# Kernel tuning notes

Measured on AMD Instinct MI355X. Metric: run time of the kernel, lower is better.

Reference implementation:

```python
import jax, jax.numpy as jnp
import numpy as np

ORDER = 2
M = 3  # number_timeseries


def setup_inputs() -> dict:
    key = jax.random.key(0)
    ks = jax.random.split(key, 8)
    N, T = 256, 4096
    H, OUT = 128, 10
    d_phi_in = (ORDER + 1) * M          # 9
    d_rho_in = ORDER * M + H            # 134
    s = lambda fan_in: 1.0 / np.sqrt(fan_in)
    return {
        "x": jax.random.normal(ks[0], (N, M * T), dtype=jnp.float32),
        "phi_w1": jax.random.normal(ks[1], (d_phi_in, H), dtype=jnp.float32) * s(d_phi_in),
        "phi_b1": jnp.zeros((H,), jnp.float32),
        "phi_w2": jax.random.normal(ks[2], (H, H), dtype=jnp.float32) * s(H),
        "phi_b2": jnp.zeros((H,), jnp.float32),
        "phi_w3": jax.random.normal(ks[3], (H, H), dtype=jnp.float32) * s(H),
        "phi_b3": jnp.zeros((H,), jnp.float32),
        "rho_w1": jax.random.normal(ks[4], (d_rho_in, H), dtype=jnp.float32) * s(d_rho_in),
        "rho_b1": jnp.zeros((H,), jnp.float32),
        "rho_w2": jax.random.normal(ks[5], (H, OUT), dtype=jnp.float32) * s(H),
        "rho_b2": jnp.zeros((OUT,), jnp.float32),
    }


def reference(x, phi_w1, phi_b1, phi_w2, phi_b2, phi_w3, phi_b3,
              rho_w1, rho_b1, rho_w2, rho_b2):
    N = x.shape[0]
    xr = x.reshape(N, M, -1)                      # (N, M, T)
    T = xr.shape[-1]
    L = T - ORDER                                 # number of windows
    # cat over lags along channel dim, then transpose -> (N, L, (ORDER+1)*M)
    input_inner = jnp.concatenate(
        [xr[:, :, i:L + i] for i in range(ORDER + 1)], axis=1
    ).swapaxes(1, 2)                              # (N, L, 9)
    h = jax.nn.relu(input_inner @ phi_w1 + phi_b1)
    h = jax.nn.relu(h @ phi_w2 + phi_b2)
    h = h @ phi_w3 + phi_b3                       # (N, L, 128)
    output_inner = jnp.sum(h, axis=1)             # (N, 128)
    input_outer = jnp.concatenate(
        [xr[:, :, :ORDER].reshape(N, -1), output_inner], axis=1
    )                                             # (N, 134)
    g = jax.nn.relu(input_outer @ rho_w1 + rho_b1)
    return g @ rho_w2 + rho_b2                    # (N, 10)
```

## Files before the change

kernel.cpp:

```cpp
#include <hip/hip_runtime.h>
#include <hip/hip_bf16.h>


#define NN 256
#define MM 3
#define TT 4096
#define LL 4094
#define HH 128
#define CHUNKS 8
#define RPC 512
#define RPH 256
#define HALVES 2
#define STEPS 4
#define SR 64
#define XROW 24

typedef __attribute__((ext_vector_type(8))) short bf16x8;
typedef __attribute__((ext_vector_type(4))) float f32x4;
typedef __attribute__((ext_vector_type(4))) unsigned short u16x4;
typedef __attribute__((ext_vector_type(2))) unsigned int u32x2;

__device__ __forceinline__ unsigned short f2bf(float x) {
    __hip_bfloat16 h = __float2bfloat16(x);
    union { __hip_bfloat16 h; unsigned short u; } v; v.h = h;
    return v.u;
}

__global__ __launch_bounds__(256, 4) void pen_inner(
    const float* __restrict__ x,
    const float* __restrict__ w1, const float* __restrict__ b1,
    const float* __restrict__ w2, const float* __restrict__ b2,
    float* __restrict__ partials)
{
    __shared__ __align__(16) unsigned short xw[XROW * (RPH + 1) + 8];
    __shared__ __align__(16) unsigned short h1s[SR * HH];

    const int tid  = threadIdx.x;
    const int wave = tid >> 6;
    const int lane = tid & 63;
    const int lr   = lane & 15;
    const int lq   = lane >> 4;

    const int bx    = blockIdx.x;
    const int n     = bx >> 3;
    const int chunk = bx & 7;
    const int l0c   = chunk * RPC;

    const float* xn = x + n * (MM * TT);

    const int fo0 = wave * 2;
    bf16x8 w1f[2];
    bf16x8 w2f[2][4];
    f32x4  b1f[2], b2f[2];
    #pragma unroll
    for (int f = 0; f < 2; ++f) {
        const int c = (fo0 + f) * 16 + lr;
        bf16x8 a;
        #pragma unroll
        for (int e = 0; e < 8; ++e) {
            int k = lq * 8 + e;
            a[e] = (short)((k < 9) ? f2bf(w1[k * HH + c]) : (unsigned short)0);
        }
        w1f[f] = a;
        #pragma unroll
        for (int kk = 0; kk < 4; ++kk) {
            bf16x8 wv;
            #pragma unroll
            for (int e = 0; e < 8; ++e)
                wv[e] = (short)f2bf(w2[(kk * 32 + lq * 8 + e) * HH + c]);
            w2f[f][kk] = wv;
        }
        #pragma unroll
        for (int j = 0; j < 4; ++j) {
            b1f[f][j] = b1[(fo0 + f) * 16 + lq * 4 + j];
            b2f[f][j] = b2[(fo0 + f) * 16 + lq * 4 + j];
        }
    }

    if (tid < XROW + 8) xw[XROW * RPH + tid] = 0;

    const int xo = XROW * lr + 8 * lq;

    float colsum[2][4] = {{0.f,0.f,0.f,0.f},{0.f,0.f,0.f,0.f}};

    for (int half = 0; half < HALVES; ++half) {
        const int lbase = l0c + half * RPH;

        {
            const int r = tid;
            unsigned short kv[9];
            #pragma unroll
            for (int k = 0; k < 9; ++k) {
                const int i = k / 3;
                const int m = k - i * 3;
                const int t = lbase + r + i;
                kv[k] = (t < TT) ? f2bf(xn[m * TT + t]) : (unsigned short)0;
            }
            u16x4 s0, s1, s2;
            s0[0] = kv[0]; s0[1] = kv[1]; s0[2] = kv[2]; s0[3] = kv[3];
            s1[0] = kv[4]; s1[1] = kv[5]; s1[2] = kv[6]; s1[3] = kv[7];
            s2[0] = kv[8]; s2[1] = 0; s2[2] = 0; s2[3] = 0;
            u16x4 z; z[0] = 0; z[1] = 0; z[2] = 0; z[3] = 0;
            *(u16x4*)&xw[XROW * r]      = s0;
            *(u16x4*)&xw[XROW * r + 4]  = s1;
            *(u16x4*)&xw[XROW * r + 8]  = s2;
            *(u16x4*)&xw[XROW * r + 12] = z;
            *(u16x4*)&xw[XROW * r + 16] = z;
            *(u16x4*)&xw[XROW * r + 20] = z;
        }

        for (int s = 0; s < STEPS; ++s) {
            __syncthreads();

            f32x4 acc1[2][4];
            #pragma unroll
            for (int rf = 0; rf < 4; ++rf) {
                bf16x8 bfrag = *(const bf16x8*)&xw[s * (XROW * SR) + rf * (XROW * 16) + xo];
                acc1[0][rf] = __builtin_amdgcn_mfma_f32_16x16x32_bf16(w1f[0], bfrag, b1f[0], 0, 0, 0);
                acc1[1][rf] = __builtin_amdgcn_mfma_f32_16x16x32_bf16(w1f[1], bfrag, b1f[1], 0, 0, 0);
            }

            #pragma unroll
            for (int rf = 0; rf < 4; ++rf) {
                const int r   = rf * 16 + lr;
                const int swz = (r & 7) << 3;
                #pragma unroll
                for (int f = 0; f < 2; ++f) {
                    const int cb = (fo0 + f) * 16 + lq * 4;
                    unsigned p0 = f2bf(fmaxf(acc1[f][rf][0], 0.f));
                    unsigned p1 = f2bf(fmaxf(acc1[f][rf][1], 0.f));
                    unsigned p2 = f2bf(fmaxf(acc1[f][rf][2], 0.f));
                    unsigned p3 = f2bf(fmaxf(acc1[f][rf][3], 0.f));
                    u32x2 pk;
                    pk[0] = p0 | (p1 << 16);
                    pk[1] = p2 | (p3 << 16);
                    *(u32x2*)&h1s[r * HH + (cb ^ swz)] = pk;
                }
            }
            __syncthreads();

            f32x4 acc2[2][4];
            #pragma unroll
            for (int rf = 0; rf < 4; ++rf) {
                const int r   = rf * 16 + lr;
                const int swz = (r & 7) << 3;
                bf16x8 hf[4];
                #pragma unroll
                for (int kk = 0; kk < 4; ++kk)
                    hf[kk] = *(const bf16x8*)&h1s[r * HH + ((kk * 32 + lq * 8) ^ swz)];
                acc2[0][rf] = __builtin_amdgcn_mfma_f32_16x16x32_bf16(w2f[0][0], hf[0], b2f[0], 0, 0, 0);
                acc2[1][rf] = __builtin_amdgcn_mfma_f32_16x16x32_bf16(w2f[1][0], hf[0], b2f[1], 0, 0, 0);
                #pragma unroll
                for (int kk = 1; kk < 4; ++kk) {
                    acc2[0][rf] = __builtin_amdgcn_mfma_f32_16x16x32_bf16(w2f[0][kk], hf[kk], acc2[0][rf], 0, 0, 0);
                    acc2[1][rf] = __builtin_amdgcn_mfma_f32_16x16x32_bf16(w2f[1][kk], hf[kk], acc2[1][rf], 0, 0, 0);
                }
            }

            const bool tailstep = (chunk == CHUNKS - 1) && (half == HALVES - 1)
                                  && (s == STEPS - 1);
            #pragma unroll
            for (int rf = 0; rf < 4; ++rf) {
                if (tailstep && rf == 3) {
                    const bool valid = lr < 14;
                    #pragma unroll
                    for (int f = 0; f < 2; ++f)
                        #pragma unroll
                        for (int j = 0; j < 4; ++j) {
                            float v = fmaxf(acc2[f][rf][j], 0.f);
                            if (valid) colsum[f][j] += v;
                        }
                } else {
                    #pragma unroll
                    for (int f = 0; f < 2; ++f)
                        #pragma unroll
                        for (int j = 0; j < 4; ++j)
                            colsum[f][j] += fmaxf(acc2[f][rf][j], 0.f);
                }
            }
        }
    }

    #pragma unroll
    for (int f = 0; f < 2; ++f)
        #pragma unroll
        for (int j = 0; j < 4; ++j) {
            float v = colsum[f][j];
            #pragma unroll
            for (int msk = 1; msk < 16; msk <<= 1)
                v += __shfl_xor(v, msk, 64);
            if (lr == 0) {
                const int o = (fo0 + f) * 16 + lq * 4 + j;
                partials[(n * CHUNKS + chunk) * HH + o] = v;
            }
        }
}

__global__ __launch_bounds__(128) void pen_outer(
    const float* __restrict__ x,
    const float* __restrict__ w3, const float* __restrict__ b3,
    const float* __restrict__ rw1, const float* __restrict__ rb1,
    const float* __restrict__ rw2, const float* __restrict__ rb2,
    const float* __restrict__ partials,
    float* __restrict__ out)
{
    __shared__ float S[HH];
    __shared__ float IO[136];
    __shared__ float G[HH];
    const int n = blockIdx.x;
    const int c = threadIdx.x;

    float s = 0.f;
    #pragma unroll
    for (int ch = 0; ch < CHUNKS; ++ch)
        s += partials[(n * CHUNKS + ch) * HH + c];
    S[c] = s;
    if (c < 6) IO[c] = x[n * (MM * TT) + (c >> 1) * TT + (c & 1)];
    __syncthreads();

    float oi = (float)LL * b3[c];
    for (int k = 0; k < HH; ++k) oi += S[k] * w3[k * HH + c];
    IO[6 + c] = oi;
    __syncthreads();

    float g = rb1[c];
    for (int k = 0; k < 134; ++k) g += IO[k] * rw1[k * HH + c];
    G[c] = fmaxf(g, 0.f);
    __syncthreads();

    if (c < 10) {
        float o = rb2[c];
        for (int k = 0; k < HH; ++k) o += G[k] * rw2[k * 10 + c];
        out[n * 10 + c] = o;
    }
}

extern "C" void kernel_launch(void* const* d_in, const int* in_sizes, int n_in,
                              void* d_out, int out_size, void* d_ws, size_t ws_size,
                              hipStream_t stream)
{
    (void)in_sizes; (void)n_in; (void)out_size; (void)ws_size;
    const float* x   = (const float*)d_in[0];
    const float* w1  = (const float*)d_in[1];
    const float* b1  = (const float*)d_in[2];
    const float* w2  = (const float*)d_in[3];
    const float* b2  = (const float*)d_in[4];
    const float* w3  = (const float*)d_in[5];
    const float* b3  = (const float*)d_in[6];
    const float* rw1 = (const float*)d_in[7];
    const float* rb1 = (const float*)d_in[8];
    const float* rw2 = (const float*)d_in[9];
    const float* rb2 = (const float*)d_in[10];

    float* partials = (float*)d_ws;

    pen_inner<<<NN * CHUNKS, 256, 0, stream>>>(x, w1, b1, w2, b2, partials);
    pen_outer<<<NN, 128, 0, stream>>>(x, w3, b3, rw1, rb1, rw2, rb2, partials,
                                      (float*)d_out);
}
```

Baseline: 73.91 us.

## Tile inner MLP as 2x2 wave grid with double-buffered hidden activations

Changes the wave decomposition from each wave owning 32 output columns across all 64 rows to a 2x2 grid where each wave owns 64 columns by 32 rows. This lets each loaded x and hidden fragment feed more MFMAs per wave. Double-buffering the h1 shared buffer removes one barrier per step, but cross-wave partial sums now need a shared-memory reduction at the end. More weight fragments live in registers, so the launch bound drops to 2 blocks per CU, which risks lower occupancy.

New measurement: 92.19 us. 1.25x slower.

```diff
diff --git a/kernel.cpp b/kernel.cpp
--- a/kernel.cpp
+++ b/kernel.cpp
@@ -26,20 +26,23 @@
     return v.u;
 }
 
-__global__ __launch_bounds__(256, 4) void pen_inner(
+__global__ __launch_bounds__(256, 2) void pen_inner(
     const float* __restrict__ x,
     const float* __restrict__ w1, const float* __restrict__ b1,
     const float* __restrict__ w2, const float* __restrict__ b2,
     float* __restrict__ partials)
 {
     __shared__ __align__(16) unsigned short xw[XROW * (RPH + 1) + 8];
-    __shared__ __align__(16) unsigned short h1s[SR * HH];
+    __shared__ __align__(16) unsigned short h1s[2][SR * HH];
+    __shared__ float red[2][HH];
 
     const int tid  = threadIdx.x;
     const int wave = tid >> 6;
     const int lane = tid & 63;
     const int lr   = lane & 15;
     const int lq   = lane >> 4;
+    const int wr   = wave >> 1;
+    const int wc   = wave & 1;
 
     const int bx    = blockIdx.x;
     const int n     = bx >> 3;
@@ -48,40 +51,37 @@
 
     const float* xn = x + n * (MM * TT);
 
-    const int fo0 = wave * 2;
-    bf16x8 w1f[2];
-    bf16x8 w2f[2][4];
-    f32x4  b1f[2], b2f[2];
+    bf16x8 w1f[4];
+    bf16x8 w2f[4][4];
+    f32x4  b1f[4], b2f[4];
     #pragma unroll
-    for (int f = 0; f < 2; ++f) {
-        const int c = (fo0 + f) * 16 + lr;
+    for (int cf = 0; cf < 4; ++cf) {
+        const int c = wc * 64 + cf * 16 + lr;
         bf16x8 a;
         #pragma unroll
         for (int e = 0; e < 8; ++e) {
             int k = lq * 8 + e;
             a[e] = (short)((k < 9) ? f2bf(w1[k * HH + c]) : (unsigned short)0);
         }
-        w1f[f] = a;
+        w1f[cf] = a;
         #pragma unroll
         for (int kk = 0; kk < 4; ++kk) {
             bf16x8 wv;
             #pragma unroll
             for (int e = 0; e < 8; ++e)
                 wv[e] = (short)f2bf(w2[(kk * 32 + lq * 8 + e) * HH + c]);
-            w2f[f][kk] = wv;
+            w2f[cf][kk] = wv;
         }
         #pragma unroll
         for (int j = 0; j < 4; ++j) {
-            b1f[f][j] = b1[(fo0 + f) * 16 + lq * 4 + j];
-            b2f[f][j] = b2[(fo0 + f) * 16 + lq * 4 + j];
+            b1f[cf][j] = b1[wc * 64 + cf * 16 + lq * 4 + j];
+            b2f[cf][j] = b2[wc * 64 + cf * 16 + lq * 4 + j];
         }
     }
 
     if (tid < XROW + 8) xw[XROW * RPH + tid] = 0;
 
-    const int xo = XROW * lr + 8 * lq;
-
-    float colsum[2][4] = {{0.f,0.f,0.f,0.f},{0.f,0.f,0.f,0.f}};
+    float colsum[4][4] = {{0,0,0,0},{0,0,0,0},{0,0,0,0},{0,0,0,0}};
 
     for (int half = 0; half < HALVES; ++half) {
         const int lbase = l0c + half * RPH;
@@ -108,92 +108,103 @@
             *(u16x4*)&xw[XROW * r + 16] = z;
             *(u16x4*)&xw[XROW * r + 20] = z;
         }
+        __syncthreads();
 
         for (int s = 0; s < STEPS; ++s) {
-            __syncthreads();
-
-            f32x4 acc1[2][4];
-            #pragma unroll
-            for (int rf = 0; rf < 4; ++rf) {
-                bf16x8 bfrag = *(const bf16x8*)&xw[s * (XROW * SR) + rf * (XROW * 16) + xo];
-                acc1[0][rf] = __builtin_amdgcn_mfma_f32_16x16x32_bf16(w1f[0], bfrag, b1f[0], 0, 0, 0);
-                acc1[1][rf] = __builtin_amdgcn_mfma_f32_16x16x32_bf16(w1f[1], bfrag, b1f[1], 0, 0, 0);
-            }
-
-            #pragma unroll
-            for (int rf = 0; rf < 4; ++rf) {
-                const int r   = rf * 16 + lr;
-                const int swz = (r & 7) << 3;
-                #pragma unroll
-                for (int f = 0; f < 2; ++f) {
-                    const int cb = (fo0 + f) * 16 + lq * 4;
-                    unsigned p0 = f2bf(fmaxf(acc1[f][rf][0], 0.f));
-                    unsigned p1 = f2bf(fmaxf(acc1[f][rf][1], 0.f));
-                    unsigned p2 = f2bf(fmaxf(acc1[f][rf][2], 0.f));
-                    unsigned p3 = f2bf(fmaxf(acc1[f][rf][3], 0.f));
+            const int buf = (half * STEPS + s) & 1;
+            unsigned short* hb = &h1s[buf][0];
+
+            bf16x8 bfr[2];
+            #pragma unroll
+            for (int rr = 0; rr < 2; ++rr) {
+                const int R = s * SR + wr * 32 + rr * 16 + lr;
+                bfr[rr] = *(const bf16x8*)&xw[R * XROW + 8 * lq];
+            }
+            f32x4 acc1[4][2];
+            #pragma unroll
+            for (int cf = 0; cf < 4; ++cf)
+                #pragma unroll
+                for (int rr = 0; rr < 2; ++rr)
+                    acc1[cf][rr] = __builtin_amdgcn_mfma_f32_16x16x32_bf16(
+                                       w1f[cf], bfr[rr], b1f[cf], 0, 0, 0);
+
+            #pragma unroll
+            for (int rr = 0; rr < 2; ++rr) {
+                const int r   = wr * 32 + rr * 16 + lr;
+                const int swz = lr << 3;
+                #pragma unroll
+                for (int cf = 0; cf < 4; ++cf) {
+                    const int cb = wc * 64 + cf * 16 + lq * 4;
+                    unsigned p0 = f2bf(fmaxf(acc1[cf][rr][0], 0.f));
+                    unsigned p1 = f2bf(fmaxf(acc1[cf][rr][1], 0.f));
+                    unsigned p2 = f2bf(fmaxf(acc1[cf][rr][2], 0.f));
+                    unsigned p3 = f2bf(fmaxf(acc1[cf][rr][3], 0.f));
                     u32x2 pk;
                     pk[0] = p0 | (p1 << 16);
                     pk[1] = p2 | (p3 << 16);
-                    *(u32x2*)&h1s[r * HH + (cb ^ swz)] = pk;
+                    *(u32x2*)&hb[r * HH + (cb ^ swz)] = pk;
                 }
             }
             __syncthreads();
 
-            f32x4 acc2[2][4];
-            #pragma unroll
-            for (int rf = 0; rf < 4; ++rf) {
-                const int r   = rf * 16 + lr;
-                const int swz = (r & 7) << 3;
+            f32x4 acc2[4][2];
+            #pragma unroll
+            for (int rr = 0; rr < 2; ++rr) {
+                const int r   = wr * 32 + rr * 16 + lr;
+                const int swz = lr << 3;
                 bf16x8 hf[4];
                 #pragma unroll
                 for (int kk = 0; kk < 4; ++kk)
-                    hf[kk] = *(const bf16x8*)&h1s[r * HH + ((kk * 32 + lq * 8) ^ swz)];
-                acc2[0][rf] = __builtin_amdgcn_mfma_f32_16x16x32_bf16(w2f[0][0], hf[0], b2f[0], 0, 0, 0);
-                acc2[1][rf] = __builtin_amdgcn_mfma_f32_16x16x32_bf16(w2f[1][0], hf[0], b2f[1], 0, 0, 0);
-                #pragma unroll
-                for (int kk = 1; kk < 4; ++kk) {
-                    acc2[0][rf] = __builtin_amdgcn_mfma_f32_16x16x32_bf16(w2f[0][kk], hf[kk], acc2[0][rf], 0, 0, 0);
-                    acc2[1][rf] = __builtin_amdgcn_mfma_f32_16x16x32_bf16(w2f[1][kk], hf[kk], acc2[1][rf], 0, 0, 0);
+                    hf[kk] = *(const bf16x8*)&hb[r * HH + ((kk * 32 + lq * 8) ^ swz)];
+                #pragma unroll
+                for (int of = 0; of < 4; ++of) {
+                    acc2[of][rr] = __builtin_amdgcn_mfma_f32_16x16x32_bf16(
+                                       w2f[of][0], hf[0], b2f[of], 0, 0, 0);
+                    #pragma unroll
+                    for (int kk = 1; kk < 4; ++kk)
+                        acc2[of][rr] = __builtin_amdgcn_mfma_f32_16x16x32_bf16(
+                                           w2f[of][kk], hf[kk], acc2[of][rr], 0, 0, 0);
                 }
             }
 
-            const bool tailstep = (chunk == CHUNKS - 1) && (half == HALVES - 1)
-                                  && (s == STEPS - 1);
-            #pragma unroll
-            for (int rf = 0; rf < 4; ++rf) {
-                if (tailstep && rf == 3) {
+            const bool tailw = (chunk == CHUNKS - 1) && (half == HALVES - 1)
+                               && (s == STEPS - 1) && (wr == 1);
+            #pragma unroll
+            for (int rr = 0; rr < 2; ++rr) {
+                if (tailw && rr == 1) {
                     const bool valid = lr < 14;
                     #pragma unroll
-                    for (int f = 0; f < 2; ++f)
+                    for (int of = 0; of < 4; ++of)
                         #pragma unroll
                         for (int j = 0; j < 4; ++j) {
-                            float v = fmaxf(acc2[f][rf][j], 0.f);
-                            if (valid) colsum[f][j] += v;
+                            float v = fmaxf(acc2[of][rr][j], 0.f);
+                            if (valid) colsum[of][j] += v;
                         }
                 } else {
                     #pragma unroll
-                    for (int f = 0; f < 2; ++f)
+                    for (int of = 0; of < 4; ++of)
                         #pragma unroll
                         for (int j = 0; j < 4; ++j)
-                            colsum[f][j] += fmaxf(acc2[f][rf][j], 0.f);
+                            colsum[of][j] += fmaxf(acc2[of][rr][j], 0.f);
                 }
             }
         }
     }
 
     #pragma unroll
-    for (int f = 0; f < 2; ++f)
+    for (int of = 0; of < 4; ++of)
         #pragma unroll
         for (int j = 0; j < 4; ++j) {
-            float v = colsum[f][j];
+            float v = colsum[of][j];
             #pragma unroll
             for (int msk = 1; msk < 16; msk <<= 1)
                 v += __shfl_xor(v, msk, 64);
-            if (lr == 0) {
-                const int o = (fo0 + f) * 16 + lq * 4 + j;
-                partials[(n * CHUNKS + chunk) * HH + o] = v;
-            }
-        }
+            if (lr == 0)
+                red[wr][wc * 64 + of * 16 + lq * 4 + j] = v;
+        }
+    __syncthreads();
+    if (tid < HH)
+        partials[(n * CHUNKS + chunk) * HH + tid] = red[0][tid] + red[1][tid];
 }
 
 __global__ __launch_bounds__(128) void pen_outer(
```
